# Performance work log

Measured on AMD Instinct MI355X. Metric: run time of the kernel, lower is better.

## Reference

```python
import jax, jax.numpy as jnp
import numpy as np

B, L, D, MAXW = 8, 512, 768, 12
H = D // 2  # forward/backward half of the bidirectional encoder output


def setup_inputs() -> dict:
    key = jax.random.key(0)
    k1, k2, k3, k4 = jax.random.split(key, 4)
    h = jax.random.normal(k1, (B, L, D), jnp.float32)
    # ATG-style span enumeration: start=i, end=min(i+w, L-1) for w in [0, MAXW)
    starts = jnp.broadcast_to(jnp.arange(L)[:, None], (L, MAXW))
    ends = jnp.minimum(starts + jnp.arange(MAXW)[None, :], L - 1)
    span_idx = jnp.stack([starts, ends], axis=-1).reshape(1, L * MAXW, 2)
    span_idx = jnp.broadcast_to(span_idx, (B, L * MAXW, 2)).astype(jnp.int64)
    # downproject: Linear(D -> D) since BidirectionalEndpointSpanExtractor output dim == D
    W = jax.random.normal(k2, (D, D), jnp.float32) / np.sqrt(D)
    b = jnp.zeros((D,), jnp.float32)
    # learned sentinels (use_sentinels=True default), one per half
    start_sentinel = jax.random.normal(k3, (H,), jnp.float32) * 0.02
    end_sentinel = jax.random.normal(k4, (H,), jnp.float32) * 0.02
    return {"h": h, "span_idx": span_idx, "W": W, "b": b,
            "start_sentinel": start_sentinel, "end_sentinel": end_sentinel}


def _gather(seq, idx):
    # seq: (B, L, H), idx: (B, S) -> (B, S, H)
    return jnp.take_along_axis(seq, idx[..., None], axis=1)


def reference(h, span_idx, W, b, start_sentinel, end_sentinel):
    Bv, Lv, Dv = h.shape
    Hv = Dv // 2
    fwd, bwd = h[..., :Hv], h[..., Hv:]
    starts = span_idx[..., 0]
    ends = span_idx[..., 1]
    # exclusive endpoints
    excl_starts = starts - 1
    start_mask = excl_starts == -1                 # before sequence start -> start sentinel
    excl_ends = ends + 1
    end_mask = excl_ends >= Lv                     # past sequence end -> end sentinel
    excl_starts = jnp.where(start_mask, 0, excl_starts)
    excl_ends = jnp.where(end_mask, 0, excl_ends)
    f_start = _gather(fwd, excl_starts)            # (B, S, H)
    f_end = _gather(fwd, ends)
    b_start = _gather(bwd, excl_ends)
    b_end = _gather(bwd, starts)
    f_start = jnp.where(start_mask[..., None], start_sentinel, f_start)
    b_start = jnp.where(end_mask[..., None], end_sentinel, b_start)
    # forward_combination='y-x', backward_combination='x-y'
    span_rep = jnp.concatenate([f_end - f_start, b_start - b_end], axis=-1)  # (B, S, D)
    out = jax.nn.relu(jnp.einsum('bsd,ed->bse', span_rep, W) + b)
    return out.reshape(Bv, Lv, -1, Dv)            # (B, L, MAXW, D)
```

## Files before the change

kernel.cpp:

```cpp
#include <hip/hip_runtime.h>

typedef __attribute__((ext_vector_type(4))) float f32x4;
typedef __attribute__((ext_vector_type(8))) _Float16 f16x8;
typedef __attribute__((ext_vector_type(4))) unsigned short u16x4;

#define NB 8
#define LLEN 512
#define DD 768
#define MW 12
#define HH 384
#define TT (NB * LLEN)
#define SS (LLEN * MW)
#define MM (2 * TT)

#define PACKH_BLOCKS ((TT * 192) / 256)
#define PACKW_BLOCKS ((DD * 192) / 256)
#define SENT_BLOCKS (DD / 4)
#define PREP_BLOCKS (PACKH_BLOCKS + PACKW_BLOCKS + SENT_BLOCKS)

__device__ __forceinline__ unsigned short f2h(float x) {
  _Float16 h = (_Float16)x;
  return __builtin_bit_cast(unsigned short, h);
}
__device__ __forceinline__ float h2f(unsigned short u) {
  return (float)__builtin_bit_cast(_Float16, u);
}
__device__ __forceinline__ void gload_lds16(const void* g, void* l) {
  __builtin_amdgcn_global_load_lds(
      (const __attribute__((address_space(1))) unsigned int*)g,
      (__attribute__((address_space(3))) unsigned int*)l, 16, 0, 0);
}

__global__ __launch_bounds__(256) void prep_k(const float* __restrict__ h,
                                              const float* __restrict__ W,
                                              const float* __restrict__ ss,
                                              const float* __restrict__ es,
                                              unsigned short* __restrict__ A,
                                              unsigned short* __restrict__ Bu,
                                              unsigned short* __restrict__ Bv,
                                              unsigned short* __restrict__ us,
                                              unsigned short* __restrict__ vs) {
  int bid = blockIdx.x;
  if (bid < PACKH_BLOCKS) {
    int idx = bid * 256 + threadIdx.x;
    int t = idx / 192;
    int k = (idx - t * 192) * 4;
    f32x4 f = *(const f32x4*)(h + (size_t)idx * 4);
    int row = (k < HH) ? t : TT + t;
    int kk = (k < HH) ? k : k - HH;
    u16x4 v;
#pragma unroll
    for (int j = 0; j < 4; ++j) v[j] = f2h(f[j]);
    *(u16x4*)(A + (size_t)row * HH + kk) = v;
  } else if (bid < PACKH_BLOCKS + PACKW_BLOCKS) {
    int idx = (bid - PACKH_BLOCKS) * 256 + threadIdx.x;
    int e = idx / 192;
    int k = (idx - e * 192) * 4;
    f32x4 f = *(const f32x4*)(W + (size_t)idx * 4);
    unsigned short* Bm = (k < HH) ? Bu : Bv;
    int kk = (k < HH) ? k : k - HH;
    u16x4 v;
#pragma unroll
    for (int j = 0; j < 4; ++j) v[j] = f2h(f[j]);
    *(u16x4*)(Bm + (size_t)e * HH + kk) = v;
  } else {
    int e = (bid - PACKH_BLOCKS - PACKW_BLOCKS) * 4 + (threadIdx.x >> 6);
    int lane = threadIdx.x & 63;
    float a = 0.f, b = 0.f;
    const float* w = W + (size_t)e * DD;
    for (int j = lane; j < HH; j += 64) {
      a += ss[j] * w[j];
      b += es[j] * w[HH + j];
    }
#pragma unroll
    for (int off = 32; off > 0; off >>= 1) {
      a += __shfl_down(a, off);
      b += __shfl_down(b, off);
    }
    if (lane == 0) { us[e] = f2h(a); vs[e] = f2h(b); }
  }
}

__global__ __launch_bounds__(256) void gemm_k(const unsigned short* __restrict__ A,
                                              const unsigned short* __restrict__ Bu,
                                              const unsigned short* __restrict__ Bv,
                                              unsigned short* __restrict__ C) {
  __shared__ unsigned short As[128 * 64];
  __shared__ unsigned short Bs[96 * 64];

  const int bid = blockIdx.x;
  const int bx = bid & 63, by = bid >> 6;
  const int tid = threadIdx.x;
  const int lane = tid & 63;
  const int w = tid >> 6;
  const int wr = w >> 1, wc = w & 1;
  const int l16 = lane & 15, l4 = lane >> 4;
  const int row0 = bx * 128;
  const int col0 = by * 96;
  const char* Bb = (const char*)((row0 < TT) ? Bu : Bv);
  const char* Ab = (const char*)A;

  f32x4 acc[4][3] = {};

  for (int kc = 0; kc < HH; kc += 64) {
#pragma unroll
    for (int r = 0; r < 4; ++r) {
      int o = (r * 256 + tid) * 16;
      int row = o >> 7, colb = o & 127;
      gload_lds16(Ab + ((size_t)(row0 + row) * HH + kc) * 2 + colb, (char*)As + o);
    }
#pragma unroll
    for (int r = 0; r < 3; ++r) {
      int o = (r * 256 + tid) * 16;
      int row = o >> 7, colb = o & 127;
      gload_lds16(Bb + ((size_t)(col0 + row) * HH + kc) * 2 + colb, (char*)Bs + o);
    }
    __syncthreads();

    f16x8 af[2][4], bf[2][3];
#pragma unroll
    for (int ks = 0; ks < 2; ++ks)
#pragma unroll
      for (int m = 0; m < 4; ++m)
        af[ks][m] = *(const f16x8*)&As[(wr * 64 + m * 16 + l16) * 64 + ks * 32 + l4 * 8];
#pragma unroll
    for (int ks = 0; ks < 2; ++ks)
#pragma unroll
      for (int n = 0; n < 3; ++n)
        bf[ks][n] = *(const f16x8*)&Bs[(wc * 48 + n * 16 + l16) * 64 + ks * 32 + l4 * 8];

#pragma unroll
    for (int m = 0; m < 4; ++m)
#pragma unroll
      for (int n = 0; n < 3; ++n) {
        acc[m][n] = __builtin_amdgcn_mfma_f32_16x16x32_f16(af[0][m], bf[0][n], acc[m][n], 0, 0, 0);
        acc[m][n] = __builtin_amdgcn_mfma_f32_16x16x32_f16(af[1][m], bf[1][n], acc[m][n], 0, 0, 0);
      }
    __syncthreads();
  }

#pragma unroll
  for (int m = 0; m < 4; ++m) {
    int grow = row0 + wr * 64 + m * 16 + l4 * 4;
#pragma unroll
    for (int n = 0; n < 3; ++n) {
      int gcol = col0 + wc * 48 + n * 16 + l16;
#pragma unroll
      for (int r = 0; r < 4; ++r)
        C[(size_t)(grow + r) * DD + gcol] = f2h(acc[m][n][r]);
    }
  }
}

__global__ __launch_bounds__(192) void assemble_k(const int* __restrict__ span,
                                                  const unsigned short* __restrict__ U,
                                                  const unsigned short* __restrict__ V,
                                                  const unsigned short* __restrict__ us,
                                                  const unsigned short* __restrict__ vs,
                                                  const float* __restrict__ bias,
                                                  float* __restrict__ out) {
  const int bid = blockIdx.x;
  const int tk = (bid & 7) * (TT / 8) + (bid >> 3);
  const int b = tk >> 9;
  const int l = tk & 511;
  const int t0 = b * LLEN;
  const int e4 = threadIdx.x;
  const u16x4* U4 = (const u16x4*)U;
  const u16x4* V4 = (const u16x4*)V;
  const f32x4 bb = ((const f32x4*)bias)[e4];
  const int2* sp = (const int2*)(span + ((size_t)b * SS + (size_t)l * MW) * 2);
  f32x4* out4 = (f32x4*)out + ((size_t)b * SS + (size_t)l * MW) * 192 + e4;

#pragma unroll 4
  for (int wdx = 0; wdx < MW; ++wdx) {
    const int2 se = sp[wdx];
    const int start = se.x, end = se.y;
    u16x4 pe = U4[(size_t)(t0 + end) * 192 + e4];
    u16x4 pv = (end + 1 >= LLEN) ? ((const u16x4*)vs)[e4]
                                 : V4[(size_t)(t0 + end + 1) * 192 + e4];
    u16x4 mu = (start == 0) ? ((const u16x4*)us)[e4]
                            : U4[(size_t)(t0 + start - 1) * 192 + e4];
    u16x4 mv = V4[(size_t)(t0 + start) * 192 + e4];
    f32x4 r;
#pragma unroll
    for (int j = 0; j < 4; ++j) {
      float x = h2f(pe[j]) + h2f(pv[j]) - h2f(mu[j]) - h2f(mv[j]) + bb[j];
      r[j] = fmaxf(x, 0.f);
    }
    out4[(size_t)wdx * 192] = r;
  }
}

__global__ __launch_bounds__(256) void naive_k(const float* __restrict__ h,
                                               const int* __restrict__ span,
                                               const float* __restrict__ W,
                                               const float* __restrict__ bias,
                                               const float* __restrict__ ss,
                                               const float* __restrict__ es,
                                               float* __restrict__ out) {
  int bs = blockIdx.x;
  int b = bs / SS;
  int start = span[(size_t)bs * 2 + 0];
  int end   = span[(size_t)bs * 2 + 1];
  __shared__ float rep[DD];
  const float* hb = h + (size_t)b * LLEN * DD;
  for (int k = threadIdx.x; k < HH; k += blockDim.x) {
    float fs = (start == 0) ? ss[k] : hb[(size_t)(start - 1) * DD + k];
    rep[k] = hb[(size_t)end * DD + k] - fs;
    float bstart = (end + 1 >= LLEN) ? es[k] : hb[(size_t)(end + 1) * DD + HH + k];
    rep[HH + k] = bstart - hb[(size_t)start * DD + HH + k];
  }
  __syncthreads();
  for (int e = threadIdx.x; e < DD; e += blockDim.x) {
    const float* w = W + (size_t)e * DD;
    float acc = bias[e];
    for (int k = 0; k < DD; k += 4) {
      acc += rep[k] * w[k] + rep[k + 1] * w[k + 1] + rep[k + 2] * w[k + 2] + rep[k + 3] * w[k + 3];
    }
    out[(size_t)bs * DD + e] = fmaxf(acc, 0.f);
  }
}

extern "C" void kernel_launch(void* const* d_in, const int* in_sizes, int n_in,
                              void* d_out, int out_size, void* d_ws, size_t ws_size,
                              hipStream_t stream) {
  const float* h  = (const float*)d_in[0];
  const int* span = (const int*)d_in[1];
  const float* W  = (const float*)d_in[2];
  const float* bias = (const float*)d_in[3];
  const float* ss = (const float*)d_in[4];
  const float* es = (const float*)d_in[5];
  float* out = (float*)d_out;

  const size_t szUV = (size_t)MM * DD * sizeof(unsigned short);
  const size_t szA  = (size_t)MM * HH * sizeof(unsigned short);
  const size_t szB  = (size_t)DD * HH * sizeof(unsigned short);
  const size_t szS  = DD * sizeof(unsigned short);
  const size_t need = szUV + szA + 2 * szB + 2 * szS;

  if (ws_size < need) {
    naive_k<<<NB * SS, 256, 0, stream>>>(h, span, W, bias, ss, es, out);
    return;
  }

  char* ws = (char*)d_ws;
  unsigned short* U  = (unsigned short*)ws;
  unsigned short* V  = U + (size_t)TT * DD;
  unsigned short* A  = (unsigned short*)(ws + szUV);
  unsigned short* Bu = A + (size_t)MM * HH;
  unsigned short* Bv = Bu + (size_t)DD * HH;
  unsigned short* us = Bv + (size_t)DD * HH;
  unsigned short* vs = us + DD;

  prep_k<<<PREP_BLOCKS, 256, 0, stream>>>(h, W, ss, es, A, Bu, Bv, us, vs);
  gemm_k<<<512, 256, 0, stream>>>(A, Bu, Bv, U);
  assemble_k<<<TT, 192, 0, stream>>>(span, U, V, us, vs, bias, out);
}
```

Baseline: 51.13 us.

## Double-buffer LDS tiles in the GEMM to overlap global loads with MFMA

The GEMM kernel now keeps two LDS buffers for its A and B tiles. It issues the direct-to-LDS loads for the next K-chunk before computing on the current one, and unrolls the six-step K loop. The aim is to hide global-memory load latency behind the MFMA work, where before each chunk was loaded and then a barrier was hit. In exchange LDS use per block doubles, which can lower occupancy. The overlap may also be lost if the compiler waits on all outstanding vector loads before the LDS reads.

New measurement: 51.44 us. About the same (+0.6%).

```diff
diff --git a/kernel.cpp b/kernel.cpp
--- a/kernel.cpp
+++ b/kernel.cpp
@@ -85,8 +85,8 @@
                                               const unsigned short* __restrict__ Bu,
                                               const unsigned short* __restrict__ Bv,
                                               unsigned short* __restrict__ C) {
-  __shared__ unsigned short As[128 * 64];
-  __shared__ unsigned short Bs[96 * 64];
+  __shared__ unsigned short As[2][128 * 64];
+  __shared__ unsigned short Bs[2][96 * 64];
 
   const int bid = blockIdx.x;
   const int bx = bid & 63, by = bid >> 6;
@@ -102,32 +102,45 @@
 
   f32x4 acc[4][3] = {};
 
-  for (int kc = 0; kc < HH; kc += 64) {
-#pragma unroll
-    for (int r = 0; r < 4; ++r) {
-      int o = (r * 256 + tid) * 16;
-      int row = o >> 7, colb = o & 127;
-      gload_lds16(Ab + ((size_t)(row0 + row) * HH + kc) * 2 + colb, (char*)As + o);
-    }
-#pragma unroll
-    for (int r = 0; r < 3; ++r) {
-      int o = (r * 256 + tid) * 16;
-      int row = o >> 7, colb = o & 127;
-      gload_lds16(Bb + ((size_t)(col0 + row) * HH + kc) * 2 + colb, (char*)Bs + o);
-    }
-    __syncthreads();
-
+#define STAGE(buf, kc)                                                          \
+  {                                                                             \
+    _Pragma("unroll")                                                           \
+    for (int r = 0; r < 4; ++r) {                                               \
+      int o = (r * 256 + tid) * 16;                                             \
+      int row = o >> 7, colb = o & 127;                                         \
+      gload_lds16(Ab + ((size_t)(row0 + row) * HH + (kc)) * 2 + colb,           \
+                  (char*)As[buf] + o);                                          \
+    }                                                                           \
+    _Pragma("unroll")                                                           \
+    for (int r = 0; r < 3; ++r) {                                               \
+      int o = (r * 256 + tid) * 16;                                             \
+      int row = o >> 7, colb = o & 127;                                         \
+      gload_lds16(Bb + ((size_t)(col0 + row) * HH + (kc)) * 2 + colb,           \
+                  (char*)Bs[buf] + o);                                          \
+    }                                                                           \
+  }
+
+  STAGE(0, 0);
+  __syncthreads();
+
+#pragma unroll
+  for (int i = 0; i < 6; ++i) {
+    const int cur = i & 1;
+    if (i < 5) STAGE(cur ^ 1, (i + 1) * 64);
+
+    const unsigned short* Ac = As[cur];
+    const unsigned short* Bc = Bs[cur];
     f16x8 af[2][4], bf[2][3];
 #pragma unroll
     for (int ks = 0; ks < 2; ++ks)
 #pragma unroll
       for (int m = 0; m < 4; ++m)
-        af[ks][m] = *(const f16x8*)&As[(wr * 64 + m * 16 + l16) * 64 + ks * 32 + l4 * 8];
+        af[ks][m] = *(const f16x8*)&Ac[(wr * 64 + m * 16 + l16) * 64 + ks * 32 + l4 * 8];
 #pragma unroll
     for (int ks = 0; ks < 2; ++ks)
 #pragma unroll
       for (int n = 0; n < 3; ++n)
-        bf[ks][n] = *(const f16x8*)&Bs[(wc * 48 + n * 16 + l16) * 64 + ks * 32 + l4 * 8];
+        bf[ks][n] = *(const f16x8*)&Bc[(wc * 48 + n * 16 + l16) * 64 + ks * 32 + l4 * 8];
 
 #pragma unroll
     for (int m = 0; m < 4; ++m)
@@ -138,6 +151,7 @@
       }
     __syncthreads();
   }
+#undef STAGE
 
 #pragma unroll
   for (int m = 0; m < 4; ++m) {
```

## Fuse projection GEMM with span assembly, keeping U/V tiles in LDS

Applied to the files above, without the earlier changes.

Merges the GEMM and assembly kernels into one. Each block computes the projected U and V rows for a 32-token chunk, with a one-row halo on each side, against a 192-wide column slice, then assembles the 12 spans per token straight from LDS. This removes the round trip of the fp16 U/V intermediate through global memory and one kernel launch. In exchange the halo rows are recomputed, and the block needs more LDS and holds a larger accumulator tile per wave.

Result: faster. 49.73 us (-2.7%).

```diff
diff --git a/kernel.cpp b/kernel.cpp
--- a/kernel.cpp
+++ b/kernel.cpp
@@ -12,6 +12,11 @@
 #define TT (NB * LLEN)
 #define SS (LLEN * MW)
 #define MM (2 * TT)
+
+#define BT 32
+#define BE 192
+#define WROWS 48
+#define PADW 204
 
 #define PACKH_BLOCKS ((TT * 192) / 256)
 #define PACKW_BLOCKS ((DD * 192) / 256)
@@ -81,113 +86,130 @@
   }
 }
 
-__global__ __launch_bounds__(256) void gemm_k(const unsigned short* __restrict__ A,
-                                              const unsigned short* __restrict__ Bu,
-                                              const unsigned short* __restrict__ Bv,
-                                              unsigned short* __restrict__ C) {
-  __shared__ unsigned short As[128 * 64];
-  __shared__ unsigned short Bs[96 * 64];
+__global__ __launch_bounds__(256) void fused_k(const unsigned short* __restrict__ A,
+                                               const unsigned short* __restrict__ Bu,
+                                               const unsigned short* __restrict__ Bv,
+                                               const int* __restrict__ span,
+                                               const unsigned short* __restrict__ us,
+                                               const unsigned short* __restrict__ vs,
+                                               const float* __restrict__ bias,
+                                               float* __restrict__ out) {
+  __shared__ char lds[96 * 64 * 2 + 2 * 192 * 64 * 2];
+  __shared__ int2 spans[BT * MW];
 
   const int bid = blockIdx.x;
-  const int bx = bid & 63, by = bid >> 6;
+  const int g = ((bid >> 5) << 3) | (bid & 7);
+  const int ec = (bid >> 3) & 3;
+  const int b = g >> 4;
+  const int tch = g & 15;
+  const int T0 = tch * BT;
+  const int E0 = ec * BE;
+
   const int tid = threadIdx.x;
   const int lane = tid & 63;
   const int w = tid >> 6;
   const int wr = w >> 1, wc = w & 1;
   const int l16 = lane & 15, l4 = lane >> 4;
-  const int row0 = bx * 128;
-  const int col0 = by * 96;
-  const char* Bb = (const char*)((row0 < TT) ? Bu : Bv);
-  const char* Ab = (const char*)A;
-
-  f32x4 acc[4][3] = {};
+
+  {
+    const int2* sp = (const int2*)span + (size_t)b * SS + (size_t)T0 * MW;
+    for (int s = tid; s < BT * MW; s += 256) spans[s] = sp[s];
+  }
+
+  unsigned short* As = (unsigned short*)lds;
+  unsigned short* Bf = As + 96 * 64;
+  unsigned short* Bb = Bf + 192 * 64;
+
+  f32x4 acc[3][6] = {};
 
   for (int kc = 0; kc < HH; kc += 64) {
-#pragma unroll
-    for (int r = 0; r < 4; ++r) {
-      int o = (r * 256 + tid) * 16;
-      int row = o >> 7, colb = o & 127;
-      gload_lds16(Ab + ((size_t)(row0 + row) * HH + kc) * 2 + colb, (char*)As + o);
-    }
 #pragma unroll
     for (int r = 0; r < 3; ++r) {
       int o = (r * 256 + tid) * 16;
-      int row = o >> 7, colb = o & 127;
-      gload_lds16(Bb + ((size_t)(col0 + row) * HH + kc) * 2 + colb, (char*)Bs + o);
+      int rr = o >> 7, colb = o & 127;
+      int tloc = T0 - 1 + (rr < WROWS ? rr : rr - WROWS);
+      tloc = min(max(tloc, 0), LLEN - 1);
+      size_t arow = (size_t)(rr < WROWS ? 0 : TT) + (size_t)b * LLEN + tloc;
+      gload_lds16((const char*)A + (arow * HH + kc) * 2 + colb, (char*)As + o);
+    }
+#pragma unroll
+    for (int r = 0; r < 6; ++r) {
+      int o = (r * 256 + tid) * 16;
+      int rr = o >> 7, colb = o & 127;
+      gload_lds16((const char*)Bu + ((size_t)(E0 + rr) * HH + kc) * 2 + colb, (char*)Bf + o);
+      gload_lds16((const char*)Bv + ((size_t)(E0 + rr) * HH + kc) * 2 + colb, (char*)Bb + o);
     }
     __syncthreads();
 
-    f16x8 af[2][4], bf[2][3];
+    const unsigned short* Am = As + (wr * WROWS) * 64;
+    const unsigned short* Bm = (wr == 0) ? Bf : Bb;
+    f16x8 af[2][3], bf[2][6];
 #pragma unroll
     for (int ks = 0; ks < 2; ++ks)
 #pragma unroll
-      for (int m = 0; m < 4; ++m)
-        af[ks][m] = *(const f16x8*)&As[(wr * 64 + m * 16 + l16) * 64 + ks * 32 + l4 * 8];
+      for (int m = 0; m < 3; ++m)
+        af[ks][m] = *(const f16x8*)&Am[(m * 16 + l16) * 64 + ks * 32 + l4 * 8];
 #pragma unroll
     for (int ks = 0; ks < 2; ++ks)
 #pragma unroll
-      for (int n = 0; n < 3; ++n)
-        bf[ks][n] = *(const f16x8*)&Bs[(wc * 48 + n * 16 + l16) * 64 + ks * 32 + l4 * 8];
-
-#pragma unroll
-    for (int m = 0; m < 4; ++m)
-#pragma unroll
-      for (int n = 0; n < 3; ++n) {
+      for (int n = 0; n < 6; ++n)
+        bf[ks][n] = *(const f16x8*)&Bm[(wc * 96 + n * 16 + l16) * 64 + ks * 32 + l4 * 8];
+
+#pragma unroll
+    for (int m = 0; m < 3; ++m)
+#pragma unroll
+      for (int n = 0; n < 6; ++n) {
         acc[m][n] = __builtin_amdgcn_mfma_f32_16x16x32_f16(af[0][m], bf[0][n], acc[m][n], 0, 0, 0);
         acc[m][n] = __builtin_amdgcn_mfma_f32_16x16x32_f16(af[1][m], bf[1][n], acc[m][n], 0, 0, 0);
       }
     __syncthreads();
   }
 
-#pragma unroll
-  for (int m = 0; m < 4; ++m) {
-    int grow = row0 + wr * 64 + m * 16 + l4 * 4;
-#pragma unroll
-    for (int n = 0; n < 3; ++n) {
-      int gcol = col0 + wc * 48 + n * 16 + l16;
-#pragma unroll
-      for (int r = 0; r < 4; ++r)
-        C[(size_t)(grow + r) * DD + gcol] = f2h(acc[m][n][r]);
-    }
-  }
-}
-
-__global__ __launch_bounds__(192) void assemble_k(const int* __restrict__ span,
-                                                  const unsigned short* __restrict__ U,
-                                                  const unsigned short* __restrict__ V,
-                                                  const unsigned short* __restrict__ us,
-                                                  const unsigned short* __restrict__ vs,
-                                                  const float* __restrict__ bias,
-                                                  float* __restrict__ out) {
-  const int bid = blockIdx.x;
-  const int tk = (bid & 7) * (TT / 8) + (bid >> 3);
-  const int b = tk >> 9;
-  const int l = tk & 511;
-  const int t0 = b * LLEN;
-  const int e4 = threadIdx.x;
-  const u16x4* U4 = (const u16x4*)U;
-  const u16x4* V4 = (const u16x4*)V;
-  const f32x4 bb = ((const f32x4*)bias)[e4];
-  const int2* sp = (const int2*)(span + ((size_t)b * SS + (size_t)l * MW) * 2);
-  f32x4* out4 = (f32x4*)out + ((size_t)b * SS + (size_t)l * MW) * 192 + e4;
-
+  unsigned short* Uld = (unsigned short*)lds;
+  unsigned short* Vld = Uld + WROWS * PADW;
+  {
+    unsigned short* Cm = (wr == 0) ? Uld : Vld;
+#pragma unroll
+    for (int m = 0; m < 3; ++m) {
+      int row = m * 16 + l4 * 4;
+#pragma unroll
+      for (int n = 0; n < 6; ++n) {
+        int col = wc * 96 + n * 16 + l16;
+#pragma unroll
+        for (int r = 0; r < 4; ++r)
+          Cm[(row + r) * PADW + col] = f2h(acc[m][n][r]);
+      }
+    }
+  }
+  __syncthreads();
+
+  const u16x4* U4 = (const u16x4*)Uld;
+  const u16x4* V4 = (const u16x4*)Vld;
+  const u16x4* us4 = (const u16x4*)us + (E0 >> 2);
+  const u16x4* vs4 = (const u16x4*)vs + (E0 >> 2);
+  const f32x4* bias4 = (const f32x4*)bias + (E0 >> 2);
+  f32x4* out4 = (f32x4*)out + ((size_t)b * SS + (size_t)T0 * MW) * (DD / 4) + (E0 >> 2);
+
+  int e4 = tid % 48;
+  int lw = tid / 48;
 #pragma unroll 4
-  for (int wdx = 0; wdx < MW; ++wdx) {
-    const int2 se = sp[wdx];
+  for (int it = 0; it < (BT * MW * 48) / 256; ++it) {
+    const int2 se = spans[lw];
     const int start = se.x, end = se.y;
-    u16x4 pe = U4[(size_t)(t0 + end) * 192 + e4];
-    u16x4 pv = (end + 1 >= LLEN) ? ((const u16x4*)vs)[e4]
-                                 : V4[(size_t)(t0 + end + 1) * 192 + e4];
-    u16x4 mu = (start == 0) ? ((const u16x4*)us)[e4]
-                            : U4[(size_t)(t0 + start - 1) * 192 + e4];
-    u16x4 mv = V4[(size_t)(t0 + start) * 192 + e4];
+    u16x4 pe = U4[(end - T0 + 1) * 51 + e4];
+    u16x4 pv = (end + 1 >= LLEN) ? vs4[e4] : V4[(end - T0 + 2) * 51 + e4];
+    u16x4 mu = (start == 0) ? us4[e4] : U4[(start - T0) * 51 + e4];
+    u16x4 mv = V4[(start - T0 + 1) * 51 + e4];
+    f32x4 bb = bias4[e4];
     f32x4 r;
 #pragma unroll
     for (int j = 0; j < 4; ++j) {
       float x = h2f(pe[j]) + h2f(pv[j]) - h2f(mu[j]) - h2f(mv[j]) + bb[j];
       r[j] = fmaxf(x, 0.f);
     }
-    out4[(size_t)wdx * 192] = r;
+    out4[(size_t)lw * (DD / 4) + e4] = r;
+    e4 += 16; lw += 5;
+    if (e4 >= 48) { e4 -= 48; lw += 1; }
   }
 }
 
@@ -232,11 +254,10 @@
   const float* es = (const float*)d_in[5];
   float* out = (float*)d_out;
 
-  const size_t szUV = (size_t)MM * DD * sizeof(unsigned short);
   const size_t szA  = (size_t)MM * HH * sizeof(unsigned short);
   const size_t szB  = (size_t)DD * HH * sizeof(unsigned short);
   const size_t szS  = DD * sizeof(unsigned short);
-  const size_t need = szUV + szA + 2 * szB + 2 * szS;
+  const size_t need = szA + 2 * szB + 2 * szS;
 
   if (ws_size < need) {
     naive_k<<<NB * SS, 256, 0, stream>>>(h, span, W, bias, ss, es, out);
@@ -244,15 +265,12 @@
   }
 
   char* ws = (char*)d_ws;
-  unsigned short* U  = (unsigned short*)ws;
-  unsigned short* V  = U + (size_t)TT * DD;
-  unsigned short* A  = (unsigned short*)(ws + szUV);
+  unsigned short* A  = (unsigned short*)ws;
   unsigned short* Bu = A + (size_t)MM * HH;
   unsigned short* Bv = Bu + (size_t)DD * HH;
   unsigned short* us = Bv + (size_t)DD * HH;
   unsigned short* vs = us + DD;
 
   prep_k<<<PREP_BLOCKS, 256, 0, stream>>>(h, W, ss, es, A, Bu, Bv, us, vs);
-  gemm_k<<<512, 256, 0, stream>>>(A, Bu, Bv, U);
-  assemble_k<<<TT, 192, 0, stream>>>(span, U, V, us, vs, bias, out);
-}
+  fused_k<<<512, 256, 0, stream>>>(A, Bu, Bv, span, us, vs, bias, out);
+}
```

## Fold fwd/bwd halves into one padded prefix-row GEMM with two-gather assembly

Applied to the files above, without the earlier changes.

Builds a padded per-batch row matrix (528 rows per batch) in which row i holds fwd[i-1] concatenated with bwd[i+1], with the sentinels filling the boundary rows. One full-K GEMM against W then yields R, and each span output becomes relu(R[end+1] - R[start] + b). The assemble kernel now does two fp16 row gathers per span instead of four, and the separate sentinel dot-product blocks are removed. The GEMM switches to K=768 with 64-row tiles and a swizzled block order, which gives fewer MFMA tiles per block. Each R row also carries the extra rows at both ends of the padded layout.

Result: no change. 51.94 us (+1.6%).

```diff
diff --git a/kernel.cpp b/kernel.cpp
--- a/kernel.cpp
+++ b/kernel.cpp
@@ -11,12 +11,12 @@
 #define HH 384
 #define TT (NB * LLEN)
 #define SS (LLEN * MW)
-#define MM (2 * TT)
-
-#define PACKH_BLOCKS ((TT * 192) / 256)
-#define PACKW_BLOCKS ((DD * 192) / 256)
-#define SENT_BLOCKS (DD / 4)
-#define PREP_BLOCKS (PACKH_BLOCKS + PACKW_BLOCKS + SENT_BLOCKS)
+#define RB 528
+#define MX (NB * RB)
+
+#define PREPX_BLOCKS ((MX * 192) / 256)
+#define PREPW_BLOCKS ((DD * 192) / 256)
+#define PREP_BLOCKS (PREPX_BLOCKS + PREPW_BLOCKS)
 
 __device__ __forceinline__ unsigned short f2h(float x) {
   _Float16 h = (_Float16)x;
@@ -35,94 +35,82 @@
                                               const float* __restrict__ W,
                                               const float* __restrict__ ss,
                                               const float* __restrict__ es,
-                                              unsigned short* __restrict__ A,
-                                              unsigned short* __restrict__ Bu,
-                                              unsigned short* __restrict__ Bv,
-                                              unsigned short* __restrict__ us,
-                                              unsigned short* __restrict__ vs) {
+                                              unsigned short* __restrict__ X,
+                                              unsigned short* __restrict__ Wp) {
   int bid = blockIdx.x;
-  if (bid < PACKH_BLOCKS) {
+  if (bid < PREPX_BLOCKS) {
     int idx = bid * 256 + threadIdx.x;
-    int t = idx / 192;
-    int k = (idx - t * 192) * 4;
-    f32x4 f = *(const f32x4*)(h + (size_t)idx * 4);
-    int row = (k < HH) ? t : TT + t;
-    int kk = (k < HH) ? k : k - HH;
+    int r = idx / 192;
+    int c = (idx - r * 192) * 4;
+    int b = r / RB;
+    int t = r - b * RB - 1;
+    const float* src;
+    if (c < HH) {
+      src = (t == -1) ? (ss + c) : (h + ((size_t)b * LLEN + min(t, LLEN - 1)) * DD + c);
+    } else {
+      src = (t >= LLEN - 1) ? (es + (c - HH))
+                            : (h + ((size_t)b * LLEN + (t + 1)) * DD + c);
+    }
+    f32x4 f = *(const f32x4*)src;
     u16x4 v;
 #pragma unroll
     for (int j = 0; j < 4; ++j) v[j] = f2h(f[j]);
-    *(u16x4*)(A + (size_t)row * HH + kk) = v;
-  } else if (bid < PACKH_BLOCKS + PACKW_BLOCKS) {
-    int idx = (bid - PACKH_BLOCKS) * 256 + threadIdx.x;
+    *(u16x4*)(X + (size_t)r * DD + c) = v;
+  } else {
+    int idx = (bid - PREPX_BLOCKS) * 256 + threadIdx.x;
     int e = idx / 192;
-    int k = (idx - e * 192) * 4;
-    f32x4 f = *(const f32x4*)(W + (size_t)idx * 4);
-    unsigned short* Bm = (k < HH) ? Bu : Bv;
-    int kk = (k < HH) ? k : k - HH;
+    int c = (idx - e * 192) * 4;
+    f32x4 f = *(const f32x4*)(W + (size_t)e * DD + c);
     u16x4 v;
 #pragma unroll
     for (int j = 0; j < 4; ++j) v[j] = f2h(f[j]);
-    *(u16x4*)(Bm + (size_t)e * HH + kk) = v;
-  } else {
-    int e = (bid - PACKH_BLOCKS - PACKW_BLOCKS) * 4 + (threadIdx.x >> 6);
-    int lane = threadIdx.x & 63;
-    float a = 0.f, b = 0.f;
-    const float* w = W + (size_t)e * DD;
-    for (int j = lane; j < HH; j += 64) {
-      a += ss[j] * w[j];
-      b += es[j] * w[HH + j];
-    }
-#pragma unroll
-    for (int off = 32; off > 0; off >>= 1) {
-      a += __shfl_down(a, off);
-      b += __shfl_down(b, off);
-    }
-    if (lane == 0) { us[e] = f2h(a); vs[e] = f2h(b); }
-  }
-}
-
-__global__ __launch_bounds__(256) void gemm_k(const unsigned short* __restrict__ A,
-                                              const unsigned short* __restrict__ Bu,
-                                              const unsigned short* __restrict__ Bv,
-                                              unsigned short* __restrict__ C) {
-  __shared__ unsigned short As[128 * 64];
+    *(u16x4*)(Wp + (size_t)e * DD + c) = v;
+  }
+}
+
+__global__ __launch_bounds__(256) void gemm_k(const unsigned short* __restrict__ X,
+                                              const unsigned short* __restrict__ Wp,
+                                              unsigned short* __restrict__ R) {
+  __shared__ unsigned short As[64 * 64];
   __shared__ unsigned short Bs[96 * 64];
 
   const int bid = blockIdx.x;
-  const int bx = bid & 63, by = bid >> 6;
+  const int sw = (bid & 7) * 66 + (bid >> 3);
+  const int mp = sw >> 3, nc = sw & 7;
+  const int r0 = mp * 64;
+  const int c0 = nc * 96;
+
   const int tid = threadIdx.x;
   const int lane = tid & 63;
   const int w = tid >> 6;
   const int wr = w >> 1, wc = w & 1;
   const int l16 = lane & 15, l4 = lane >> 4;
-  const int row0 = bx * 128;
-  const int col0 = by * 96;
-  const char* Bb = (const char*)((row0 < TT) ? Bu : Bv);
-  const char* Ab = (const char*)A;
-
-  f32x4 acc[4][3] = {};
-
-  for (int kc = 0; kc < HH; kc += 64) {
-#pragma unroll
-    for (int r = 0; r < 4; ++r) {
+  const char* Xb = (const char*)X;
+  const char* Wb = (const char*)Wp;
+
+  f32x4 acc[2][3] = {};
+
+  for (int kc = 0; kc < DD; kc += 64) {
+#pragma unroll
+    for (int r = 0; r < 2; ++r) {
       int o = (r * 256 + tid) * 16;
-      int row = o >> 7, colb = o & 127;
-      gload_lds16(Ab + ((size_t)(row0 + row) * HH + kc) * 2 + colb, (char*)As + o);
+      int rr = o >> 7, colb = o & 127;
+      gload_lds16(Xb + ((size_t)(r0 + rr) * DD + kc) * 2 + colb, (char*)As + o);
     }
 #pragma unroll
     for (int r = 0; r < 3; ++r) {
       int o = (r * 256 + tid) * 16;
-      int row = o >> 7, colb = o & 127;
-      gload_lds16(Bb + ((size_t)(col0 + row) * HH + kc) * 2 + colb, (char*)Bs + o);
+      int rr = o >> 7, colb = o & 127;
+      gload_lds16(Wb + ((size_t)(c0 + rr) * DD + kc) * 2 + colb, (char*)Bs + o);
     }
     __syncthreads();
 
-    f16x8 af[2][4], bf[2][3];
+    f16x8 af[2][2], bf[2][3];
 #pragma unroll
     for (int ks = 0; ks < 2; ++ks)
 #pragma unroll
-      for (int m = 0; m < 4; ++m)
-        af[ks][m] = *(const f16x8*)&As[(wr * 64 + m * 16 + l16) * 64 + ks * 32 + l4 * 8];
+      for (int m = 0; m < 2; ++m)
+        af[ks][m] = *(const f16x8*)&As[(wr * 32 + m * 16 + l16) * 64 + ks * 32 + l4 * 8];
 #pragma unroll
     for (int ks = 0; ks < 2; ++ks)
 #pragma unroll
@@ -130,7 +118,7 @@
         bf[ks][n] = *(const f16x8*)&Bs[(wc * 48 + n * 16 + l16) * 64 + ks * 32 + l4 * 8];
 
 #pragma unroll
-    for (int m = 0; m < 4; ++m)
+    for (int m = 0; m < 2; ++m)
 #pragma unroll
       for (int n = 0; n < 3; ++n) {
         acc[m][n] = __builtin_amdgcn_mfma_f32_16x16x32_f16(af[0][m], bf[0][n], acc[m][n], 0, 0, 0);
@@ -140,33 +128,29 @@
   }
 
 #pragma unroll
-  for (int m = 0; m < 4; ++m) {
-    int grow = row0 + wr * 64 + m * 16 + l4 * 4;
+  for (int m = 0; m < 2; ++m) {
+    int grow = r0 + wr * 32 + m * 16 + l4 * 4;
 #pragma unroll
     for (int n = 0; n < 3; ++n) {
-      int gcol = col0 + wc * 48 + n * 16 + l16;
+      int gcol = c0 + wc * 48 + n * 16 + l16;
 #pragma unroll
       for (int r = 0; r < 4; ++r)
-        C[(size_t)(grow + r) * DD + gcol] = f2h(acc[m][n][r]);
+        R[(size_t)(grow + r) * DD + gcol] = f2h(acc[m][n][r]);
     }
   }
 }
 
 __global__ __launch_bounds__(192) void assemble_k(const int* __restrict__ span,
-                                                  const unsigned short* __restrict__ U,
-                                                  const unsigned short* __restrict__ V,
-                                                  const unsigned short* __restrict__ us,
-                                                  const unsigned short* __restrict__ vs,
+                                                  const unsigned short* __restrict__ R,
                                                   const float* __restrict__ bias,
                                                   float* __restrict__ out) {
   const int bid = blockIdx.x;
   const int tk = (bid & 7) * (TT / 8) + (bid >> 3);
   const int b = tk >> 9;
   const int l = tk & 511;
-  const int t0 = b * LLEN;
+  const int base = b * RB;
   const int e4 = threadIdx.x;
-  const u16x4* U4 = (const u16x4*)U;
-  const u16x4* V4 = (const u16x4*)V;
+  const u16x4* R4 = (const u16x4*)R;
   const f32x4 bb = ((const f32x4*)bias)[e4];
   const int2* sp = (const int2*)(span + ((size_t)b * SS + (size_t)l * MW) * 2);
   f32x4* out4 = (f32x4*)out + ((size_t)b * SS + (size_t)l * MW) * 192 + e4;
@@ -174,17 +158,12 @@
 #pragma unroll 4
   for (int wdx = 0; wdx < MW; ++wdx) {
     const int2 se = sp[wdx];
-    const int start = se.x, end = se.y;
-    u16x4 pe = U4[(size_t)(t0 + end) * 192 + e4];
-    u16x4 pv = (end + 1 >= LLEN) ? ((const u16x4*)vs)[e4]
-                                 : V4[(size_t)(t0 + end + 1) * 192 + e4];
-    u16x4 mu = (start == 0) ? ((const u16x4*)us)[e4]
-                            : U4[(size_t)(t0 + start - 1) * 192 + e4];
-    u16x4 mv = V4[(size_t)(t0 + start) * 192 + e4];
+    u16x4 pe = R4[(size_t)(base + se.y + 1) * 192 + e4];
+    u16x4 mq = R4[(size_t)(base + se.x) * 192 + e4];
     f32x4 r;
 #pragma unroll
     for (int j = 0; j < 4; ++j) {
-      float x = h2f(pe[j]) + h2f(pv[j]) - h2f(mu[j]) - h2f(mv[j]) + bb[j];
+      float x = h2f(pe[j]) - h2f(mq[j]) + bb[j];
       r[j] = fmaxf(x, 0.f);
     }
     out4[(size_t)wdx * 192] = r;
@@ -232,11 +211,10 @@
   const float* es = (const float*)d_in[5];
   float* out = (float*)d_out;
 
-  const size_t szUV = (size_t)MM * DD * sizeof(unsigned short);
-  const size_t szA  = (size_t)MM * HH * sizeof(unsigned short);
-  const size_t szB  = (size_t)DD * HH * sizeof(unsigned short);
-  const size_t szS  = DD * sizeof(unsigned short);
-  const size_t need = szUV + szA + 2 * szB + 2 * szS;
+  const size_t szX = (size_t)MX * DD * sizeof(unsigned short);
+  const size_t szW = (size_t)DD * DD * sizeof(unsigned short);
+  const size_t szR = (size_t)MX * DD * sizeof(unsigned short);
+  const size_t need = szX + szW + szR;
 
   if (ws_size < need) {
     naive_k<<<NB * SS, 256, 0, stream>>>(h, span, W, bias, ss, es, out);
@@ -244,15 +222,11 @@
   }
 
   char* ws = (char*)d_ws;
-  unsigned short* U  = (unsigned short*)ws;
-  unsigned short* V  = U + (size_t)TT * DD;
-  unsigned short* A  = (unsigned short*)(ws + szUV);
-  unsigned short* Bu = A + (size_t)MM * HH;
-  unsigned short* Bv = Bu + (size_t)DD * HH;
-  unsigned short* us = Bv + (size_t)DD * HH;
-  unsigned short* vs = us + DD;
-
-  prep_k<<<PREP_BLOCKS, 256, 0, stream>>>(h, W, ss, es, A, Bu, Bv, us, vs);
-  gemm_k<<<512, 256, 0, stream>>>(A, Bu, Bv, U);
-  assemble_k<<<TT, 192, 0, stream>>>(span, U, V, us, vs, bias, out);
-}
+  unsigned short* X  = (unsigned short*)ws;
+  unsigned short* Wp = X + (size_t)MX * DD;
+  unsigned short* R  = Wp + (size_t)DD * DD;
+
+  prep_k<<<PREP_BLOCKS, 256, 0, stream>>>(h, W, ss, es, X, Wp);
+  gemm_k<<<528, 256, 0, stream>>>(X, Wp, R);
+  assemble_k<<<TT, 192, 0, stream>>>(span, R, bias, out);
+}
```
